# Kernel tuning notes

Hardware: AMD Instinct MI355X
Metric: run time of the kernel (lower is better)

Reference implementation:

```python
import jax, jax.numpy as jnp
import numpy as np

B, T, D, H, BAND = 2, 4096, 512, 8, 16
LN_EPS = 1e-5


def setup_inputs() -> dict:
    key = jax.random.key(0)
    k0, k1, k2 = jax.random.split(key, 3)
    x = jax.random.normal(k0, (B, T, D), jnp.float32)
    # nn.MultiheadAttention params: packed in_proj [3D, D] and out_proj [D, D]
    w_in = jax.random.normal(k1, (3 * D, D), jnp.float32) * 0.02
    b_in = jnp.zeros((3 * D,), jnp.float32)
    w_out = jax.random.normal(k2, (D, D), jnp.float32) * 0.02
    b_out = jnp.zeros((D,), jnp.float32)
    ln_g = jnp.ones((D,), jnp.float32)
    ln_b = jnp.zeros((D,), jnp.float32)
    return dict(x=x, ln_g=ln_g, ln_b=ln_b, w_in=w_in, b_in=b_in,
                w_out=w_out, b_out=b_out)


def reference(x, ln_g, ln_b, w_in, b_in, w_out, b_out):
    Bq, Tq, Dq = x.shape
    dh = Dq // H
    # LayerNorm
    mu = jnp.mean(x, axis=-1, keepdims=True)
    var = jnp.mean(jnp.square(x - mu), axis=-1, keepdims=True)
    h = (x - mu) * jax.lax.rsqrt(var + LN_EPS) * ln_g + ln_b
    # packed QKV projection (torch Linear: y = h @ W^T + b)
    qkv = h @ w_in.T + b_in                      # [B, T, 3D]
    q, k, v = jnp.split(qkv, 3, axis=-1)
    to_heads = lambda a: a.reshape(Bq, Tq, H, dh).transpose(0, 2, 1, 3)  # [B,H,T,dh]
    q, k, v = to_heads(q), to_heads(k), to_heads(v)
    # band-gather: each query t attends to keys in [t-BAND, t+BAND]
    Wn = 2 * BAND + 1
    offs = jnp.arange(-BAND, BAND + 1)
    idx = jnp.arange(Tq)[:, None] + offs[None, :]          # [T, Wn]
    valid = (idx >= 0) & (idx < Tq)                        # [T, Wn]
    idx_c = jnp.clip(idx, 0, Tq - 1)
    k_win = k[:, :, idx_c]                                 # [B,H,T,Wn,dh]
    v_win = v[:, :, idx_c]                                 # [B,H,T,Wn,dh]
    scale = 1.0 / np.sqrt(dh).astype(np.float32)
    scores = jnp.einsum('bhtd,bhtwd->bhtw', q * scale, k_win)
    scores = jnp.where(valid[None, None], scores, -jnp.inf)
    p = jax.nn.softmax(scores, axis=-1)                    # [B,H,T,Wn]
    o = jnp.einsum('bhtw,bhtwd->bhtd', p, v_win)           # [B,H,T,dh]
    o = o.transpose(0, 2, 1, 3).reshape(Bq, Tq, Dq)
    y = o @ w_out.T + b_out
    return x + y
```

## Files before the change

### kernel.cpp

```cpp
#include <hip/hip_runtime.h>
#include <hip/hip_bf16.h>

#define T_ 4096
#define D_ 512
#define H_ 8
#define BAND 16
#define G1_K 512
#define G1_NT 8

typedef float f32x4 __attribute__((ext_vector_type(4)));
typedef __bf16 bf16x8 __attribute__((ext_vector_type(8)));
typedef unsigned short us8 __attribute__((ext_vector_type(8)));
typedef unsigned short us4 __attribute__((ext_vector_type(4)));

__device__ __forceinline__ unsigned short f2b(float f) {
  union { float f; unsigned u; } v; v.f = f;
  unsigned r = v.u + 0x7fffu + ((v.u >> 16) & 1u);
  return (unsigned short)(r >> 16);
}

__device__ __forceinline__ f32x4 mfma16(bf16x8 a, bf16x8 b, f32x4 c) {
  return __builtin_amdgcn_mfma_f32_16x16x32_bf16(a, b, c, 0, 0, 0);
}

#define GLD16(gp, lp) __builtin_amdgcn_global_load_lds( \
    (const __attribute__((address_space(1))) void*)(gp), \
    (__attribute__((address_space(3))) void*)(lp), 16, 0, 0)

__global__ __launch_bounds__(256) void prep_k(const float* __restrict__ x,
                                              const float* __restrict__ g,
                                              const float* __restrict__ bt,
                                              const float* __restrict__ win,
                                              const float* __restrict__ wout,
                                              unsigned short* __restrict__ h,
                                              unsigned short* __restrict__ winb,
                                              unsigned short* __restrict__ woutb) {
  int bx = blockIdx.x;
  if (bx >= 2048) {
    int i = (bx - 2048) * 256 + threadIdx.x;
    const int n1 = 3 * D_ * D_ / 4;
    if (i < n1) {
      float4 v = ((const float4*)win)[i];
      us4 o; o.x = f2b(v.x); o.y = f2b(v.y); o.z = f2b(v.z); o.w = f2b(v.w);
      ((us4*)winb)[i] = o;
    } else {
      int j = i - n1;
      float4 v = ((const float4*)wout)[j];
      us4 o; o.x = f2b(v.x); o.y = f2b(v.y); o.z = f2b(v.z); o.w = f2b(v.w);
      ((us4*)woutb)[j] = o;
    }
    return;
  }
  int wave = threadIdx.x >> 6, lane = threadIdx.x & 63;
  size_t row = (size_t)bx * 4 + wave;
  const float4* xr = (const float4*)(x + row * D_);
  float4 a = xr[lane * 2], b = xr[lane * 2 + 1];
  float s = a.x + a.y + a.z + a.w + b.x + b.y + b.z + b.w;
  #pragma unroll
  for (int o = 32; o; o >>= 1) s += __shfl_xor(s, o, 64);
  float mu = s * (1.0f / D_);
  float d0 = a.x - mu, d1 = a.y - mu, d2 = a.z - mu, d3 = a.w - mu;
  float d4 = b.x - mu, d5 = b.y - mu, d6 = b.z - mu, d7 = b.w - mu;
  float q = d0*d0 + d1*d1 + d2*d2 + d3*d3 + d4*d4 + d5*d5 + d6*d6 + d7*d7;
  #pragma unroll
  for (int o = 32; o; o >>= 1) q += __shfl_xor(q, o, 64);
  float rstd = rsqrtf(q * (1.0f / D_) + 1e-5f);
  const float4* gr = (const float4*)g;
  const float4* br = (const float4*)bt;
  float4 g0 = gr[lane * 2], g1 = gr[lane * 2 + 1];
  float4 b0 = br[lane * 2], b1 = br[lane * 2 + 1];
  us8 o8;
  o8[0] = f2b(d0 * rstd * g0.x + b0.x);
  o8[1] = f2b(d1 * rstd * g0.y + b0.y);
  o8[2] = f2b(d2 * rstd * g0.z + b0.z);
  o8[3] = f2b(d3 * rstd * g0.w + b0.w);
  o8[4] = f2b(d4 * rstd * g1.x + b1.x);
  o8[5] = f2b(d5 * rstd * g1.y + b1.y);
  o8[6] = f2b(d6 * rstd * g1.z + b1.z);
  o8[7] = f2b(d7 * rstd * g1.w + b1.w);
  *((us8*)(h + row * D_) + lane) = o8;
}

#define OPA 0
#define OPB 1

__device__ __forceinline__ void stg(const unsigned short* __restrict__ gb,
                                    unsigned short* lds, int slot, int op, int h, int tt,
                                    int rl0, int u0, int su) {
  #pragma unroll
  for (int j = 0; j < 2; ++j) {
    const unsigned short* g = gb + (size_t)(h * 128 + rl0 + 64 * j) * G1_K + tt * 64 + su;
    unsigned short* lp = lds + slot * 32768 + op * 16384 + h * 8192 + (rl0 + 64 * j) * 64 + u0 * 8;
    GLD16(g, lp);
  }
}

#define VMC4 asm volatile("s_waitcnt vmcnt(4)" ::: "memory")
#define VMC0 asm volatile("s_waitcnt vmcnt(0)" ::: "memory")

#define PHASE(SLOT, PH, STAGE_STMT, WAIT_STMT) do {                                        \
    if ((PH) == 0) {                                                                       \
      _Pragma("unroll") for (int nf = 0; nf < 4; ++nf) {                                   \
        breg[nf][0] = *(const bf16x8*)(lds + (SLOT)*32768 + boff + nf*1024 + swz0);        \
        breg[nf][1] = *(const bf16x8*)(lds + (SLOT)*32768 + boff + nf*1024 + swz1);        \
      }                                                                                    \
    }                                                                                      \
    bf16x8 a0k0 = *(const bf16x8*)(lds + (SLOT)*32768 + aoff + (2*(PH))*1024 + swz0);      \
    bf16x8 a0k1 = *(const bf16x8*)(lds + (SLOT)*32768 + aoff + (2*(PH))*1024 + swz1);      \
    bf16x8 a1k0 = *(const bf16x8*)(lds + (SLOT)*32768 + aoff + (2*(PH)+1)*1024 + swz0);    \
    bf16x8 a1k1 = *(const bf16x8*)(lds + (SLOT)*32768 + aoff + (2*(PH)+1)*1024 + swz1);    \
    STAGE_STMT;                                                                            \
    __builtin_amdgcn_s_barrier();                                                          \
    asm volatile("s_waitcnt lgkmcnt(0)" ::: "memory");                                     \
    __builtin_amdgcn_sched_barrier(0);                                                     \
    __builtin_amdgcn_s_setprio(1);                                                         \
    _Pragma("unroll") for (int nf = 0; nf < 4; ++nf) {                                     \
      acc[2*(PH)][nf]   = mfma16(a0k0, breg[nf][0], acc[2*(PH)][nf]);                      \
      acc[2*(PH)][nf]   = mfma16(a0k1, breg[nf][1], acc[2*(PH)][nf]);                      \
      acc[2*(PH)+1][nf] = mfma16(a1k0, breg[nf][0], acc[2*(PH)+1][nf]);                    \
      acc[2*(PH)+1][nf] = mfma16(a1k1, breg[nf][1], acc[2*(PH)+1][nf]);                    \
    }                                                                                      \
    __builtin_amdgcn_s_setprio(0);                                                         \
    __builtin_amdgcn_sched_barrier(0);                                                     \
    WAIT_STMT;                                                                             \
    __builtin_amdgcn_s_barrier();                                                          \
  } while (0)

__global__ __launch_bounds__(512, 2) void gemm_qkv8(const unsigned short* __restrict__ A,
                                                    const unsigned short* __restrict__ Bw,
                                                    const float* __restrict__ bias,
                                                    unsigned short* __restrict__ C) {
  extern __shared__ char smem[];
  unsigned short* lds = (unsigned short*)smem;
  int tid = threadIdx.x;
  int lane = tid & 63, wave = tid >> 6;
  int wm = wave >> 2, wn = wave & 3;
  int fr = lane & 15, fq = lane >> 4;
  int d = blockIdx.x;
  int l = (d & 7) * 24 + (d >> 3);
  int bm = l / 6, bn = l % 6;

  const unsigned short* Ag = A + (size_t)bm * 256 * G1_K;
  const unsigned short* Bg = Bw + (size_t)bn * 256 * G1_K;

  int rl0 = tid >> 3, u0 = tid & 7;
  int su = (u0 ^ (rl0 & 7)) * 8;

  int aoff = wm * 8192 + fr * 64;
  int boff = 16384 + (wn >> 1) * 8192 + ((wn & 1) * 64 + fr) * 64;
  int swz0 = (fq ^ (fr & 7)) * 8;
  int swz1 = ((4 + fq) ^ (fr & 7)) * 8;

  f32x4 acc[8][4] = {};
  bf16x8 breg[4][2];

  stg(Bg, lds, 0, OPB, 0, 0, rl0, u0, su);
  stg(Bg, lds, 0, OPB, 1, 0, rl0, u0, su);
  stg(Ag, lds, 0, OPA, 0, 0, rl0, u0, su);
  stg(Ag, lds, 0, OPA, 1, 0, rl0, u0, su);
  stg(Bg, lds, 1, OPB, 0, 1, rl0, u0, su);
  stg(Bg, lds, 1, OPB, 1, 1, rl0, u0, su);
  VMC4;
  __builtin_amdgcn_s_barrier();

  #pragma unroll 1
  for (int i = 0; i < 3; ++i) {
    int t = 2 * i;
    PHASE(0, 0, stg(Ag, lds, 1, OPA, 0, t + 1, rl0, u0, su), (void)0);
    PHASE(0, 1, stg(Ag, lds, 1, OPA, 1, t + 1, rl0, u0, su), (void)0);
    PHASE(0, 2, stg(Bg, lds, 0, OPB, 0, t + 2, rl0, u0, su), (void)0);
    PHASE(0, 3, stg(Bg, lds, 0, OPB, 1, t + 2, rl0, u0, su), VMC4);
    PHASE(1, 0, stg(Ag, lds, 0, OPA, 0, t + 2, rl0, u0, su), (void)0);
    PHASE(1, 1, stg(Ag, lds, 0, OPA, 1, t + 2, rl0, u0, su), (void)0);
    PHASE(1, 2, stg(Bg, lds, 1, OPB, 0, t + 3, rl0, u0, su), (void)0);
    PHASE(1, 3, stg(Bg, lds, 1, OPB, 1, t + 3, rl0, u0, su), VMC4);
  }
  PHASE(0, 0, stg(Ag, lds, 1, OPA, 0, 7, rl0, u0, su), (void)0);
  PHASE(0, 1, stg(Ag, lds, 1, OPA, 1, 7, rl0, u0, su), (void)0);
  PHASE(0, 2, (void)0, (void)0);
  PHASE(0, 3, (void)0, VMC0);
  PHASE(1, 0, (void)0, (void)0);
  PHASE(1, 1, (void)0, (void)0);
  PHASE(1, 2, (void)0, (void)0);
  PHASE(1, 3, (void)0, (void)0);

  int rbase = bm * 256 + wm * 128 + fq * 4;
  int cbase = bn * 256 + wn * 64 + fr;
  float bv[4];
  #pragma unroll
  for (int nf = 0; nf < 4; ++nf) bv[nf] = bias[cbase + nf * 16];
  #pragma unroll
  for (int mf = 0; mf < 8; ++mf)
    #pragma unroll
    for (int nf = 0; nf < 4; ++nf)
      #pragma unroll
      for (int r = 0; r < 4; ++r)
        C[(size_t)(rbase + mf * 16 + r) * 1536 + cbase + nf * 16] = f2b(acc[mf][nf][r] + bv[nf]);
}

__global__ __launch_bounds__(256) void gemm_bt2(const unsigned short* __restrict__ A,
                                                const unsigned short* __restrict__ Bw,
                                                const float* __restrict__ bias,
                                                const float* __restrict__ xres,
                                                float* __restrict__ ofp,
                                                int N, int K) {
  __shared__ unsigned short As[128 * 64];
  __shared__ unsigned short Bs[128 * 64];
  int tid = threadIdx.x;
  int lane = tid & 63;
  int wave = tid >> 6;
  int wm = wave >> 1, wn = wave & 1;
  int fr = lane & 15, fq = lane >> 4;
  int dd = blockIdx.x;
  int nbn = N >> 7;
  int l = (dd & 7) * (gridDim.x >> 3) + (dd >> 3);
  int bm = l / nbn, bn = l % nbn;

  const unsigned short* Ap[4];
  const unsigned short* Bp[4];
  int loff[4];
  #pragma unroll
  for (int g = 0; g < 4; ++g) {
    int s = g * 256 + tid;
    int row = s >> 3, u = s & 7;
    int uu = u ^ (row & 7);
    Ap[g] = A + (size_t)(bm * 128 + row) * K + uu * 8;
    Bp[g] = Bw + (size_t)(bn * 128 + row) * K + uu * 8;
    loff[g] = s * 16;
  }

  f32x4 acc[4][4] = {};

  int nk = K >> 6;
  for (int kt = 0; kt < nk; ++kt) {
    int ko = kt * 64;
    #pragma unroll
    for (int g = 0; g < 4; ++g) GLD16(Ap[g] + ko, (char*)As + loff[g]);
    #pragma unroll
    for (int g = 0; g < 4; ++g) GLD16(Bp[g] + ko, (char*)Bs + loff[g]);
    __syncthreads();
    #pragma unroll
    for (int kk = 0; kk < 2; ++kk) {
      bf16x8 af[4], bfr[4];
      #pragma unroll
      for (int i = 0; i < 4; ++i) {
        int row = wm * 64 + i * 16 + fr;
        af[i] = *(const bf16x8*)(As + row * 64 + (((kk * 4 + fq) ^ (fr & 7)) << 3));
      }
      #pragma unroll
      for (int j = 0; j < 4; ++j) {
        int row = wn * 64 + j * 16 + fr;
        bfr[j] = *(const bf16x8*)(Bs + row * 64 + (((kk * 4 + fq) ^ (fr & 7)) << 3));
      }
      #pragma unroll
      for (int i = 0; i < 4; ++i)
        #pragma unroll
        for (int j = 0; j < 4; ++j)
          acc[i][j] = mfma16(af[i], bfr[j], acc[i][j]);
    }
    __syncthreads();
  }

  int rbase = bm * 128 + wm * 64 + fq * 4;
  int cb = bn * 128 + wn * 64 + fr;
  #pragma unroll
  for (int j = 0; j < 4; ++j) {
    int col = cb + j * 16;
    float bvv = bias[col];
    #pragma unroll
    for (int i = 0; i < 4; ++i) {
      #pragma unroll
      for (int r = 0; r < 4; ++r) {
        size_t idx = (size_t)(rbase + i * 16 + r) * N + col;
        ofp[idx] = xres[idx] + acc[i][j][r] + bvv;
      }
    }
  }
}

__global__ __launch_bounds__(256) void attn_k(const unsigned short* __restrict__ qkv,
                                              unsigned short* __restrict__ obuf) {
  __shared__ unsigned short Ks[96 * 72];
  __shared__ unsigned short Vt[64 * 128];
  __shared__ unsigned short Ps[64 * 104];
  int tid = threadIdx.x;
  int lane = tid & 63, wave = tid >> 6;
  int fr = lane & 15, fq = lane >> 4;
  int t0 = blockIdx.x * 64;
  int hh = blockIdx.y;
  int bb = blockIdx.z;
  size_t rowbase = (size_t)bb * T_;

  #pragma unroll
  for (int it = 0; it < 3; ++it) {
    int c = tid + it * 256;
    int r = c >> 3;
    int u = c & 7;
    int d8 = u * 8;
    int tg = t0 - BAND + r;
    us8 kv = {0,0,0,0,0,0,0,0}, vv = {0,0,0,0,0,0,0,0};
    if (tg >= 0 && tg < T_) {
      const unsigned short* p = qkv + (rowbase + tg) * 1536 + hh * 64 + d8;
      kv = *(const us8*)(p + 512);
      vv = *(const us8*)(p + 1024);
    }
    *(us8*)(Ks + r * 72 + d8) = kv;
    int ru = r >> 3, rl = r & 7;
    #pragma unroll
    for (int j = 0; j < 8; ++j)
      Vt[(d8 + j) * 128 + (((ru ^ u) << 3) | rl)] = vv[j];
  }

  bf16x8 qf0, qf1;
  {
    int tq = t0 + wave * 16 + fr;
    const unsigned short* qp = qkv + (rowbase + tq) * 1536 + hh * 64 + fq * 8;
    qf0 = *(const bf16x8*)qp;
    qf1 = *(const bf16x8*)(qp + 32);
  }
  __syncthreads();

  f32x4 sa[6];
  #pragma unroll
  for (int c = 0; c < 6; ++c) sa[c] = (f32x4){0.f, 0.f, 0.f, 0.f};
  #pragma unroll
  for (int c = 0; c < 6; ++c) {
    bf16x8 k0 = *(const bf16x8*)(Ks + (c * 16 + fr) * 72 + fq * 8);
    bf16x8 k1 = *(const bf16x8*)(Ks + (c * 16 + fr) * 72 + 32 + fq * 8);
    sa[c] = mfma16(qf0, k0, sa[c]);
    sa[c] = mfma16(qf1, k1, sa[c]);
  }

  float inv[4];
  float pvv[6][4];
  #pragma unroll
  for (int r = 0; r < 4; ++r) {
    int tg = t0 + wave * 16 + fq * 4 + r;
    float m = -1e30f;
    #pragma unroll
    for (int c = 0; c < 6; ++c) {
      int cg = t0 - BAND + c * 16 + fr;
      bool ok = (cg >= tg - BAND) && (cg <= tg + BAND) && (cg >= 0) && (cg < T_);
      float v = ok ? sa[c][r] * 0.125f : -1e30f;
      pvv[c][r] = v;
      m = fmaxf(m, v);
    }
    #pragma unroll
    for (int o = 8; o; o >>= 1) m = fmaxf(m, __shfl_xor(m, o, 64));
    float s = 0.0f;
    #pragma unroll
    for (int c = 0; c < 6; ++c) {
      float e = exp2f((pvv[c][r] - m) * 1.44269504f);
      pvv[c][r] = e;
      s += e;
    }
    #pragma unroll
    for (int o = 8; o; o >>= 1) s += __shfl_xor(s, o, 64);
    inv[r] = 1.0f / s;
  }

  #pragma unroll
  for (int c = 0; c < 6; ++c)
    #pragma unroll
    for (int r = 0; r < 4; ++r)
      Ps[(wave * 16 + fq * 4 + r) * 104 + c * 16 + fr] = f2b(pvv[c][r]);

  __syncthreads();

  f32x4 oa[4];
  #pragma unroll
  for (int c2 = 0; c2 < 4; ++c2) oa[c2] = (f32x4){0.f, 0.f, 0.f, 0.f};
  #pragma unroll
  for (int kk = 0; kk < 3; ++kk) {
    bf16x8 pa = *(const bf16x8*)(Ps + (wave * 16 + fr) * 104 + kk * 32 + fq * 8);
    #pragma unroll
    for (int c2 = 0; c2 < 4; ++c2) {
      int drow = c2 * 16 + fr;
      int ud = (drow >> 3) & 7;
      bf16x8 vb = *(const bf16x8*)(Vt + drow * 128 + (((kk * 4 + fq) ^ ud) << 3));
      oa[c2] = mfma16(pa, vb, oa[c2]);
    }
  }

  size_t orow = rowbase + t0 + wave * 16 + fq * 4;
  #pragma unroll
  for (int c2 = 0; c2 < 4; ++c2)
    #pragma unroll
    for (int r = 0; r < 4; ++r)
      obuf[(orow + r) * D_ + hh * 64 + c2 * 16 + fr] = f2b(oa[c2][r] * inv[r]);
}

extern "C" void kernel_launch(void* const* d_in, const int* in_sizes, int n_in,
                              void* d_out, int out_size, void* d_ws, size_t ws_size,
                              hipStream_t stream) {
  (void)in_sizes; (void)n_in; (void)out_size; (void)ws_size;
  const float* x     = (const float*)d_in[0];
  const float* ln_g  = (const float*)d_in[1];
  const float* ln_b  = (const float*)d_in[2];
  const float* w_in  = (const float*)d_in[3];
  const float* b_in  = (const float*)d_in[4];
  const float* w_out = (const float*)d_in[5];
  const float* b_out = (const float*)d_in[6];
  float* out = (float*)d_out;

  char* ws = (char*)d_ws;
  unsigned short* hb    = (unsigned short*)(ws);
  unsigned short* winb  = (unsigned short*)(ws + 8388608);
  unsigned short* woutb = (unsigned short*)(ws + 9961472);
  unsigned short* qkvb  = (unsigned short*)(ws + 10485760);
  unsigned short* obf   = (unsigned short*)(ws + 35651584);

  (void)hipFuncSetAttribute((const void*)gemm_qkv8,
                            hipFuncAttributeMaxDynamicSharedMemorySize, 131072);

  prep_k<<<3072, 256, 0, stream>>>(x, ln_g, ln_b, w_in, w_out, hb, winb, woutb);
  gemm_qkv8<<<192, 512, 131072, stream>>>(hb, winb, b_in, qkvb);
  attn_k<<<dim3(64, 8, 2), 256, 0, stream>>>(qkvb, obf);
  gemm_bt2<<<256, 256, 0, stream>>>(obf, woutb, b_out, x, out, 512, 512);
}
```

Before: 61.93 us.

## Fuse banded attention with output projection into one kernel

Replaces the separate attention kernel and output-projection GEMM with one kernel. Each block of 32 rows computes attention for all 8 heads, two passes of 4 heads each, into an LDS tile, then multiplies that tile by W_out with B fragments read straight from global memory. The residual add and bias are applied in the same kernel. This removes the bf16 attention-output round trip through global memory and one kernel launch. In exchange, each block redundantly reloads the K/V halo, and with only 256 blocks of 512 threads using about 114KB of LDS, parallelism and occupancy are lower.

New measurement: 61.77 us. No clear change (-0.3%).

```diff
diff --git a/kernel.cpp b/kernel.cpp
--- a/kernel.cpp
+++ b/kernel.cpp
@@ -6,7 +6,6 @@
 #define H_ 8
 #define BAND 16
 #define G1_K 512
-#define G1_NT 8
 
 typedef float f32x4 __attribute__((ext_vector_type(4)));
 typedef __bf16 bf16x8 __attribute__((ext_vector_type(8)));
@@ -198,196 +197,168 @@
         C[(size_t)(rbase + mf * 16 + r) * 1536 + cbase + nf * 16] = f2b(acc[mf][nf][r] + bv[nf]);
 }
 
-__global__ __launch_bounds__(256) void gemm_bt2(const unsigned short* __restrict__ A,
-                                                const unsigned short* __restrict__ Bw,
-                                                const float* __restrict__ bias,
-                                                const float* __restrict__ xres,
-                                                float* __restrict__ ofp,
-                                                int N, int K) {
-  __shared__ unsigned short As[128 * 64];
-  __shared__ unsigned short Bs[128 * 64];
-  int tid = threadIdx.x;
-  int lane = tid & 63;
-  int wave = tid >> 6;
-  int wm = wave >> 1, wn = wave & 1;
-  int fr = lane & 15, fq = lane >> 4;
-  int dd = blockIdx.x;
-  int nbn = N >> 7;
-  int l = (dd & 7) * (gridDim.x >> 3) + (dd >> 3);
-  int bm = l / nbn, bn = l % nbn;
-
-  const unsigned short* Ap[4];
-  const unsigned short* Bp[4];
-  int loff[4];
-  #pragma unroll
-  for (int g = 0; g < 4; ++g) {
-    int s = g * 256 + tid;
-    int row = s >> 3, u = s & 7;
-    int uu = u ^ (row & 7);
-    Ap[g] = A + (size_t)(bm * 128 + row) * K + uu * 8;
-    Bp[g] = Bw + (size_t)(bn * 128 + row) * K + uu * 8;
-    loff[g] = s * 16;
-  }
-
-  f32x4 acc[4][4] = {};
-
-  int nk = K >> 6;
-  for (int kt = 0; kt < nk; ++kt) {
-    int ko = kt * 64;
-    #pragma unroll
-    for (int g = 0; g < 4; ++g) GLD16(Ap[g] + ko, (char*)As + loff[g]);
-    #pragma unroll
-    for (int g = 0; g < 4; ++g) GLD16(Bp[g] + ko, (char*)Bs + loff[g]);
-    __syncthreads();
-    #pragma unroll
-    for (int kk = 0; kk < 2; ++kk) {
-      bf16x8 af[4], bfr[4];
-      #pragma unroll
-      for (int i = 0; i < 4; ++i) {
-        int row = wm * 64 + i * 16 + fr;
-        af[i] = *(const bf16x8*)(As + row * 64 + (((kk * 4 + fq) ^ (fr & 7)) << 3));
-      }
-      #pragma unroll
-      for (int j = 0; j < 4; ++j) {
-        int row = wn * 64 + j * 16 + fr;
-        bfr[j] = *(const bf16x8*)(Bs + row * 64 + (((kk * 4 + fq) ^ (fr & 7)) << 3));
-      }
-      #pragma unroll
-      for (int i = 0; i < 4; ++i)
-        #pragma unroll
-        for (int j = 0; j < 4; ++j)
-          acc[i][j] = mfma16(af[i], bfr[j], acc[i][j]);
-    }
-    __syncthreads();
-  }
-
-  int rbase = bm * 128 + wm * 64 + fq * 4;
-  int cb = bn * 128 + wn * 64 + fr;
-  #pragma unroll
-  for (int j = 0; j < 4; ++j) {
-    int col = cb + j * 16;
-    float bvv = bias[col];
-    #pragma unroll
-    for (int i = 0; i < 4; ++i) {
-      #pragma unroll
-      for (int r = 0; r < 4; ++r) {
-        size_t idx = (size_t)(rbase + i * 16 + r) * N + col;
-        ofp[idx] = xres[idx] + acc[i][j][r] + bvv;
-      }
-    }
-  }
-}
-
-__global__ __launch_bounds__(256) void attn_k(const unsigned short* __restrict__ qkv,
-                                              unsigned short* __restrict__ obuf) {
-  __shared__ unsigned short Ks[96 * 72];
-  __shared__ unsigned short Vt[64 * 128];
-  __shared__ unsigned short Ps[64 * 104];
+__global__ __launch_bounds__(512, 2) void attn_out_k(const unsigned short* __restrict__ qkv,
+                                                     const unsigned short* __restrict__ woutb,
+                                                     const float* __restrict__ bout,
+                                                     const float* __restrict__ x,
+                                                     float* __restrict__ out) {
+  extern __shared__ char smem2[];
+  unsigned short* lds = (unsigned short*)smem2;
   int tid = threadIdx.x;
   int lane = tid & 63, wave = tid >> 6;
   int fr = lane & 15, fq = lane >> 4;
-  int t0 = blockIdx.x * 64;
-  int hh = blockIdx.y;
-  int bb = blockIdx.z;
+  int r0g = blockIdx.x * 32;
+  int bb = r0g >> 12;
+  int t0 = r0g & (T_ - 1);
   size_t rowbase = (size_t)bb * T_;
 
-  #pragma unroll
-  for (int it = 0; it < 3; ++it) {
-    int c = tid + it * 256;
-    int r = c >> 3;
-    int u = c & 7;
-    int d8 = u * 8;
-    int tg = t0 - BAND + r;
-    us8 kv = {0,0,0,0,0,0,0,0}, vv = {0,0,0,0,0,0,0,0};
-    if (tg >= 0 && tg < T_) {
-      const unsigned short* p = qkv + (rowbase + tg) * 1536 + hh * 64 + d8;
-      kv = *(const us8*)(p + 512);
-      vv = *(const us8*)(p + 1024);
-    }
-    *(us8*)(Ks + r * 72 + d8) = kv;
-    int ru = r >> 3, rl = r & 7;
-    #pragma unroll
-    for (int j = 0; j < 8; ++j)
-      Vt[(d8 + j) * 128 + (((ru ^ u) << 3) | rl)] = vv[j];
-  }
-
-  bf16x8 qf0, qf1;
-  {
-    int tq = t0 + wave * 16 + fr;
-    const unsigned short* qp = qkv + (rowbase + tq) * 1536 + hh * 64 + fq * 8;
-    qf0 = *(const bf16x8*)qp;
-    qf1 = *(const bf16x8*)(qp + 32);
-  }
-  __syncthreads();
-
-  f32x4 sa[6];
-  #pragma unroll
-  for (int c = 0; c < 6; ++c) sa[c] = (f32x4){0.f, 0.f, 0.f, 0.f};
-  #pragma unroll
-  for (int c = 0; c < 6; ++c) {
-    bf16x8 k0 = *(const bf16x8*)(Ks + (c * 16 + fr) * 72 + fq * 8);
-    bf16x8 k1 = *(const bf16x8*)(Ks + (c * 16 + fr) * 72 + 32 + fq * 8);
-    sa[c] = mfma16(qf0, k0, sa[c]);
-    sa[c] = mfma16(qf1, k1, sa[c]);
-  }
-
-  float inv[4];
-  float pvv[6][4];
-  #pragma unroll
-  for (int r = 0; r < 4; ++r) {
-    int tg = t0 + wave * 16 + fq * 4 + r;
-    float m = -1e30f;
-    #pragma unroll
-    for (int c = 0; c < 6; ++c) {
-      int cg = t0 - BAND + c * 16 + fr;
-      bool ok = (cg >= tg - BAND) && (cg <= tg + BAND) && (cg >= 0) && (cg < T_);
-      float v = ok ? sa[c][r] * 0.125f : -1e30f;
-      pvv[c][r] = v;
-      m = fmaxf(m, v);
-    }
-    #pragma unroll
-    for (int o = 8; o; o >>= 1) m = fmaxf(m, __shfl_xor(m, o, 64));
-    float s = 0.0f;
-    #pragma unroll
-    for (int c = 0; c < 6; ++c) {
-      float e = exp2f((pvv[c][r] - m) * 1.44269504f);
-      pvv[c][r] = e;
-      s += e;
-    }
-    #pragma unroll
-    for (int o = 8; o; o >>= 1) s += __shfl_xor(s, o, 64);
-    inv[r] = 1.0f / s;
-  }
-
-  #pragma unroll
-  for (int c = 0; c < 6; ++c)
-    #pragma unroll
-    for (int r = 0; r < 4; ++r)
-      Ps[(wave * 16 + fq * 4 + r) * 104 + c * 16 + fr] = f2b(pvv[c][r]);
-
-  __syncthreads();
-
-  f32x4 oa[4];
-  #pragma unroll
-  for (int c2 = 0; c2 < 4; ++c2) oa[c2] = (f32x4){0.f, 0.f, 0.f, 0.f};
-  #pragma unroll
-  for (int kk = 0; kk < 3; ++kk) {
-    bf16x8 pa = *(const bf16x8*)(Ps + (wave * 16 + fr) * 104 + kk * 32 + fq * 8);
-    #pragma unroll
-    for (int c2 = 0; c2 < 4; ++c2) {
-      int drow = c2 * 16 + fr;
-      int ud = (drow >> 3) & 7;
-      bf16x8 vb = *(const bf16x8*)(Vt + drow * 128 + (((kk * 4 + fq) ^ ud) << 3));
-      oa[c2] = mfma16(pa, vb, oa[c2]);
-    }
-  }
-
-  size_t orow = rowbase + t0 + wave * 16 + fq * 4;
-  #pragma unroll
-  for (int c2 = 0; c2 < 4; ++c2)
-    #pragma unroll
-    for (int r = 0; r < 4; ++r)
-      obuf[(orow + r) * D_ + hh * 64 + c2 * 16 + fr] = f2b(oa[c2][r] * inv[r]);
+  unsigned short* Ob = lds + 41984;
+
+  #pragma unroll 1
+  for (int rd = 0; rd < 2; ++rd) {
+    #pragma unroll
+    for (int i = 0; i < 8; ++i) {
+      int idx = i * 512 + tid;
+      int s   = idx >> 10;
+      int rem = idx & 1023;
+      int ten = rem >> 9;
+      int c   = rem & 511;
+      int r   = c >> 3, u = c & 7;
+      int hh  = 4 * rd + s;
+      int tg  = t0 - BAND + r;
+      us8 v8 = {0, 0, 0, 0, 0, 0, 0, 0};
+      if (tg >= 0 && tg < T_)
+        v8 = *(const us8*)(qkv + (rowbase + tg) * 1536 + (ten ? 1024 : 512) + hh * 64 + u * 8);
+      if (ten == 0) {
+        *(us8*)(lds + s * 8192 + r * 64 + ((u ^ (r & 7)) << 3)) = v8;
+      } else {
+        int base = s * 8192 + 4096;
+        #pragma unroll
+        for (int j = 0; j < 8; ++j)
+          lds[base + (u * 8 + j) * 64 + (((r >> 3) ^ u) << 3) + (r & 7)] = v8[j];
+      }
+    }
+    __syncthreads();
+
+    {
+      int s  = wave >> 1;
+      int hh = 4 * rd + s;
+      int qg = wave & 1;
+      int q  = t0 + qg * 16 + fr;
+
+      const unsigned short* qp = qkv + (rowbase + q) * 1536 + hh * 64;
+      bf16x8 qf0 = *(const bf16x8*)(qp + fq * 8);
+      bf16x8 qf1 = *(const bf16x8*)(qp + 32 + fq * 8);
+
+      const unsigned short* Kb = lds + s * 8192;
+      f32x4 sacc[4];
+      #pragma unroll
+      for (int mf = 0; mf < 4; ++mf) sacc[mf] = (f32x4){0.f, 0.f, 0.f, 0.f};
+      #pragma unroll
+      for (int mf = 0; mf < 4; ++mf) {
+        bf16x8 k0 = *(const bf16x8*)(Kb + (mf * 16 + fr) * 64 + ((fq ^ (fr & 7)) << 3));
+        bf16x8 k1 = *(const bf16x8*)(Kb + (mf * 16 + fr) * 64 + (((4 + fq) ^ (fr & 7)) << 3));
+        sacc[mf] = mfma16(k0, qf0, sacc[mf]);
+        sacc[mf] = mfma16(k1, qf1, sacc[mf]);
+      }
+
+      float ev[4][4];
+      float vmx = -1e30f;
+      #pragma unroll
+      for (int mf = 0; mf < 4; ++mf)
+        #pragma unroll
+        for (int r = 0; r < 4; ++r) {
+          int tk = t0 - BAND + mf * 16 + fq * 4 + r;
+          bool ok = (tk >= q - BAND) && (tk <= q + BAND) && (tk >= 0) && (tk < T_);
+          float v = ok ? sacc[mf][r] * 0.125f : -1e30f;
+          ev[mf][r] = v;
+          vmx = fmaxf(vmx, v);
+        }
+      vmx = fmaxf(vmx, __shfl_xor(vmx, 16, 64));
+      vmx = fmaxf(vmx, __shfl_xor(vmx, 32, 64));
+      float ssum = 0.f;
+      #pragma unroll
+      for (int mf = 0; mf < 4; ++mf)
+        #pragma unroll
+        for (int r = 0; r < 4; ++r) {
+          float e = (ev[mf][r] > -1e29f) ? exp2f((ev[mf][r] - vmx) * 1.44269504f) : 0.f;
+          ev[mf][r] = e;
+          ssum += e;
+        }
+      ssum += __shfl_xor(ssum, 16, 64);
+      ssum += __shfl_xor(ssum, 32, 64);
+      float inv = 1.0f / ssum;
+
+      unsigned short* Pb = lds + 32768 + wave * 1152;
+      #pragma unroll
+      for (int mf = 0; mf < 4; ++mf)
+        #pragma unroll
+        for (int r = 0; r < 4; ++r)
+          Pb[fr * 72 + mf * 16 + fq * 4 + r] = f2b(ev[mf][r] * inv);
+      asm volatile("s_waitcnt lgkmcnt(0)" ::: "memory");
+      __builtin_amdgcn_sched_barrier(0);
+
+      const unsigned short* Vb = lds + s * 8192 + 4096;
+      f32x4 oacc[4];
+      #pragma unroll
+      for (int cf = 0; cf < 4; ++cf) oacc[cf] = (f32x4){0.f, 0.f, 0.f, 0.f};
+      #pragma unroll
+      for (int kk = 0; kk < 2; ++kk) {
+        bf16x8 pa = *(const bf16x8*)(Pb + fr * 72 + (kk * 4 + fq) * 8);
+        #pragma unroll
+        for (int cf = 0; cf < 4; ++cf) {
+          int du = cf * 2 + (fr >> 3);
+          bf16x8 vf = *(const bf16x8*)(Vb + (cf * 16 + fr) * 64 + (((kk * 4 + fq) ^ du) << 3));
+          oacc[cf] = mfma16(pa, vf, oacc[cf]);
+        }
+      }
+
+      #pragma unroll
+      for (int cf = 0; cf < 4; ++cf)
+        #pragma unroll
+        for (int r = 0; r < 4; ++r) {
+          int qq = qg * 16 + fq * 4 + r;
+          int unit = hh * 8 + (((cf * 2 + (fr >> 3)) ^ (qq & 7)));
+          Ob[qq * 512 + unit * 8 + (fr & 7)] = f2b(oacc[cf][r]);
+        }
+    }
+    __syncthreads();
+  }
+
+  f32x4 acc[2][4];
+  #pragma unroll
+  for (int mf = 0; mf < 2; ++mf)
+    #pragma unroll
+    for (int nf = 0; nf < 4; ++nf) acc[mf][nf] = (f32x4){0.f, 0.f, 0.f, 0.f};
+
+  const unsigned short* Bb = woutb + (size_t)(wave * 64) * 512;
+  #pragma unroll 4
+  for (int ks = 0; ks < 16; ++ks) {
+    bf16x8 a0 = *(const bf16x8*)(Ob + (0 * 16 + fr) * 512 + (((ks * 4 + fq) ^ (fr & 7)) << 3));
+    bf16x8 a1 = *(const bf16x8*)(Ob + (1 * 16 + fr) * 512 + (((ks * 4 + fq) ^ (fr & 7)) << 3));
+    bf16x8 bfr[4];
+    #pragma unroll
+    for (int nf = 0; nf < 4; ++nf)
+      bfr[nf] = *(const bf16x8*)(Bb + (size_t)(nf * 16 + fr) * 512 + ks * 32 + fq * 8);
+    #pragma unroll
+    for (int nf = 0; nf < 4; ++nf) {
+      acc[0][nf] = mfma16(a0, bfr[nf], acc[0][nf]);
+      acc[1][nf] = mfma16(a1, bfr[nf], acc[1][nf]);
+    }
+  }
+
+  #pragma unroll
+  for (int mf = 0; mf < 2; ++mf)
+    #pragma unroll
+    for (int nf = 0; nf < 4; ++nf) {
+      int col = wave * 64 + nf * 16 + fr;
+      float bv = bout[col];
+      #pragma unroll
+      for (int r = 0; r < 4; ++r) {
+        size_t e = (size_t)(r0g + mf * 16 + fq * 4 + r) * 512 + col;
+        out[e] = x[e] + acc[mf][nf][r] + bv;
+      }
+    }
 }
 
 extern "C" void kernel_launch(void* const* d_in, const int* in_sizes, int n_in,
@@ -408,13 +379,13 @@
   unsigned short* winb  = (unsigned short*)(ws + 8388608);
   unsigned short* woutb = (unsigned short*)(ws + 9961472);
   unsigned short* qkvb  = (unsigned short*)(ws + 10485760);
-  unsigned short* obf   = (unsigned short*)(ws + 35651584);
 
   (void)hipFuncSetAttribute((const void*)gemm_qkv8,
                             hipFuncAttributeMaxDynamicSharedMemorySize, 131072);
+  (void)hipFuncSetAttribute((const void*)attn_out_k,
+                            hipFuncAttributeMaxDynamicSharedMemorySize, 116736);
 
   prep_k<<<3072, 256, 0, stream>>>(x, ln_g, ln_b, w_in, w_out, hb, winb, woutb);
   gemm_qkv8<<<192, 512, 131072, stream>>>(hb, winb, b_in, qkvb);
-  attn_k<<<dim3(64, 8, 2), 256, 0, stream>>>(qkvb, obf);
-  gemm_bt2<<<256, 256, 0, stream>>>(obf, woutb, b_out, x, out, 512, 512);
-}
+  attn_out_k<<<256, 512, 116736, stream>>>(qkvb, woutb, b_out, x, out);
+}
```

## Retile QKV GEMM to 256x192 tiles for 256 blocks; simplify attention V layout

Applied to the files above, without the earlier changes.

The QKV GEMM tile changes from 256x256 to 256x192, so the grid grows from 192 to 256 blocks and fills all 256 CUs of the MI355X. B staging, the LDS slot size, the vmcnt waits and the block-to-tile mapping are reworked to match. Each block now does less MFMA work per staged A tile, which lowers arithmetic intensity. Separately, the attention kernel drops the XOR-swizzled transposed V layout for a padded stride-104 layout and adds an occupancy hint, which may introduce LDS bank conflicts.

Result: faster. 56.62 us (-8.6%).

```diff
diff --git a/kernel.cpp b/kernel.cpp
--- a/kernel.cpp
+++ b/kernel.cpp
@@ -6,7 +6,6 @@
 #define H_ 8
 #define BAND 16
 #define G1_K 512
-#define G1_NT 8
 
 typedef float f32x4 __attribute__((ext_vector_type(4)));
 typedef __bf16 bf16x8 __attribute__((ext_vector_type(8)));
@@ -81,40 +80,47 @@
   *((us8*)(h + row * D_) + lane) = o8;
 }
 
-#define OPA 0
-#define OPB 1
-
-__device__ __forceinline__ void stg(const unsigned short* __restrict__ gb,
-                                    unsigned short* lds, int slot, int op, int h, int tt,
-                                    int rl0, int u0, int su) {
+#define SLOT_SZ 28672
+
+__device__ __forceinline__ void stgA(const unsigned short* __restrict__ gb,
+                                     unsigned short* lds, int slot, int h, int tt,
+                                     int rl0, int u0, int su) {
   #pragma unroll
   for (int j = 0; j < 2; ++j) {
-    const unsigned short* g = gb + (size_t)(h * 128 + rl0 + 64 * j) * G1_K + tt * 64 + su;
-    unsigned short* lp = lds + slot * 32768 + op * 16384 + h * 8192 + (rl0 + 64 * j) * 64 + u0 * 8;
-    GLD16(g, lp);
-  }
-}
-
-#define VMC4 asm volatile("s_waitcnt vmcnt(4)" ::: "memory")
+    int row = h * 128 + rl0 + 64 * j;
+    GLD16(gb + (size_t)row * G1_K + tt * 64 + su, lds + slot * SLOT_SZ + row * 64 + u0 * 8);
+  }
+}
+__device__ __forceinline__ void stgB(const unsigned short* __restrict__ gb,
+                                     unsigned short* lds, int slot, int tt,
+                                     int rl0, int u0, int su) {
+  #pragma unroll
+  for (int c = 0; c < 3; ++c) {
+    int row = c * 64 + rl0;
+    GLD16(gb + (size_t)row * G1_K + tt * 64 + su, lds + slot * SLOT_SZ + 16384 + row * 64 + u0 * 8);
+  }
+}
+
+#define VMC3 asm volatile("s_waitcnt vmcnt(3)" ::: "memory")
 #define VMC0 asm volatile("s_waitcnt vmcnt(0)" ::: "memory")
 
 #define PHASE(SLOT, PH, STAGE_STMT, WAIT_STMT) do {                                        \
     if ((PH) == 0) {                                                                       \
-      _Pragma("unroll") for (int nf = 0; nf < 4; ++nf) {                                   \
-        breg[nf][0] = *(const bf16x8*)(lds + (SLOT)*32768 + boff + nf*1024 + swz0);        \
-        breg[nf][1] = *(const bf16x8*)(lds + (SLOT)*32768 + boff + nf*1024 + swz1);        \
+      _Pragma("unroll") for (int nf = 0; nf < 3; ++nf) {                                   \
+        breg[nf][0] = *(const bf16x8*)(lds + (SLOT)*SLOT_SZ + boff + nf*1024 + swz0);      \
+        breg[nf][1] = *(const bf16x8*)(lds + (SLOT)*SLOT_SZ + boff + nf*1024 + swz1);      \
       }                                                                                    \
     }                                                                                      \
-    bf16x8 a0k0 = *(const bf16x8*)(lds + (SLOT)*32768 + aoff + (2*(PH))*1024 + swz0);      \
-    bf16x8 a0k1 = *(const bf16x8*)(lds + (SLOT)*32768 + aoff + (2*(PH))*1024 + swz1);      \
-    bf16x8 a1k0 = *(const bf16x8*)(lds + (SLOT)*32768 + aoff + (2*(PH)+1)*1024 + swz0);    \
-    bf16x8 a1k1 = *(const bf16x8*)(lds + (SLOT)*32768 + aoff + (2*(PH)+1)*1024 + swz1);    \
+    bf16x8 a0k0 = *(const bf16x8*)(lds + (SLOT)*SLOT_SZ + aoff + (2*(PH))*1024 + swz0);    \
+    bf16x8 a0k1 = *(const bf16x8*)(lds + (SLOT)*SLOT_SZ + aoff + (2*(PH))*1024 + swz1);    \
+    bf16x8 a1k0 = *(const bf16x8*)(lds + (SLOT)*SLOT_SZ + aoff + (2*(PH)+1)*1024 + swz0);  \
+    bf16x8 a1k1 = *(const bf16x8*)(lds + (SLOT)*SLOT_SZ + aoff + (2*(PH)+1)*1024 + swz1);  \
     STAGE_STMT;                                                                            \
     __builtin_amdgcn_s_barrier();                                                          \
     asm volatile("s_waitcnt lgkmcnt(0)" ::: "memory");                                     \
     __builtin_amdgcn_sched_barrier(0);                                                     \
     __builtin_amdgcn_s_setprio(1);                                                         \
-    _Pragma("unroll") for (int nf = 0; nf < 4; ++nf) {                                     \
+    _Pragma("unroll") for (int nf = 0; nf < 3; ++nf) {                                     \
       acc[2*(PH)][nf]   = mfma16(a0k0, breg[nf][0], acc[2*(PH)][nf]);                      \
       acc[2*(PH)][nf]   = mfma16(a0k1, breg[nf][1], acc[2*(PH)][nf]);                      \
       acc[2*(PH)+1][nf] = mfma16(a1k0, breg[nf][0], acc[2*(PH)+1][nf]);                    \
@@ -137,46 +143,44 @@
   int wm = wave >> 2, wn = wave & 3;
   int fr = lane & 15, fq = lane >> 4;
   int d = blockIdx.x;
-  int l = (d & 7) * 24 + (d >> 3);
-  int bm = l / 6, bn = l % 6;
+  int l = (d & 7) * 32 + (d >> 3);
+  int bm = l >> 3, bn = l & 7;
 
   const unsigned short* Ag = A + (size_t)bm * 256 * G1_K;
-  const unsigned short* Bg = Bw + (size_t)bn * 256 * G1_K;
+  const unsigned short* Bg = Bw + (size_t)bn * 192 * G1_K;
 
   int rl0 = tid >> 3, u0 = tid & 7;
   int su = (u0 ^ (rl0 & 7)) * 8;
 
   int aoff = wm * 8192 + fr * 64;
-  int boff = 16384 + (wn >> 1) * 8192 + ((wn & 1) * 64 + fr) * 64;
+  int boff = 16384 + (wn * 48 + fr) * 64;
   int swz0 = (fq ^ (fr & 7)) * 8;
   int swz1 = ((4 + fq) ^ (fr & 7)) * 8;
 
-  f32x4 acc[8][4] = {};
-  bf16x8 breg[4][2];
-
-  stg(Bg, lds, 0, OPB, 0, 0, rl0, u0, su);
-  stg(Bg, lds, 0, OPB, 1, 0, rl0, u0, su);
-  stg(Ag, lds, 0, OPA, 0, 0, rl0, u0, su);
-  stg(Ag, lds, 0, OPA, 1, 0, rl0, u0, su);
-  stg(Bg, lds, 1, OPB, 0, 1, rl0, u0, su);
-  stg(Bg, lds, 1, OPB, 1, 1, rl0, u0, su);
-  VMC4;
+  f32x4 acc[8][3] = {};
+  bf16x8 breg[3][2];
+
+  stgB(Bg, lds, 0, 0, rl0, u0, su);
+  stgA(Ag, lds, 0, 0, 0, rl0, u0, su);
+  stgA(Ag, lds, 0, 1, 0, rl0, u0, su);
+  stgB(Bg, lds, 1, 1, rl0, u0, su);
+  VMC3;
   __builtin_amdgcn_s_barrier();
 
   #pragma unroll 1
   for (int i = 0; i < 3; ++i) {
     int t = 2 * i;
-    PHASE(0, 0, stg(Ag, lds, 1, OPA, 0, t + 1, rl0, u0, su), (void)0);
-    PHASE(0, 1, stg(Ag, lds, 1, OPA, 1, t + 1, rl0, u0, su), (void)0);
-    PHASE(0, 2, stg(Bg, lds, 0, OPB, 0, t + 2, rl0, u0, su), (void)0);
-    PHASE(0, 3, stg(Bg, lds, 0, OPB, 1, t + 2, rl0, u0, su), VMC4);
-    PHASE(1, 0, stg(Ag, lds, 0, OPA, 0, t + 2, rl0, u0, su), (void)0);
-    PHASE(1, 1, stg(Ag, lds, 0, OPA, 1, t + 2, rl0, u0, su), (void)0);
-    PHASE(1, 2, stg(Bg, lds, 1, OPB, 0, t + 3, rl0, u0, su), (void)0);
-    PHASE(1, 3, stg(Bg, lds, 1, OPB, 1, t + 3, rl0, u0, su), VMC4);
-  }
-  PHASE(0, 0, stg(Ag, lds, 1, OPA, 0, 7, rl0, u0, su), (void)0);
-  PHASE(0, 1, stg(Ag, lds, 1, OPA, 1, 7, rl0, u0, su), (void)0);
+    PHASE(0, 0, stgA(Ag, lds, 1, 0, t + 1, rl0, u0, su), (void)0);
+    PHASE(0, 1, stgA(Ag, lds, 1, 1, t + 1, rl0, u0, su), (void)0);
+    PHASE(0, 2, stgB(Bg, lds, 0, t + 2, rl0, u0, su), (void)0);
+    PHASE(0, 3, (void)0, VMC3);
+    PHASE(1, 0, stgA(Ag, lds, 0, 0, t + 2, rl0, u0, su), (void)0);
+    PHASE(1, 1, stgA(Ag, lds, 0, 1, t + 2, rl0, u0, su), (void)0);
+    PHASE(1, 2, stgB(Bg, lds, 1, t + 3, rl0, u0, su), (void)0);
+    PHASE(1, 3, (void)0, VMC3);
+  }
+  PHASE(0, 0, stgA(Ag, lds, 1, 0, 7, rl0, u0, su), (void)0);
+  PHASE(0, 1, stgA(Ag, lds, 1, 1, 7, rl0, u0, su), (void)0);
   PHASE(0, 2, (void)0, (void)0);
   PHASE(0, 3, (void)0, VMC0);
   PHASE(1, 0, (void)0, (void)0);
@@ -185,14 +189,14 @@
   PHASE(1, 3, (void)0, (void)0);
 
   int rbase = bm * 256 + wm * 128 + fq * 4;
-  int cbase = bn * 256 + wn * 64 + fr;
-  float bv[4];
-  #pragma unroll
-  for (int nf = 0; nf < 4; ++nf) bv[nf] = bias[cbase + nf * 16];
+  int cbase = bn * 192 + wn * 48 + fr;
+  float bv[3];
+  #pragma unroll
+  for (int nf = 0; nf < 3; ++nf) bv[nf] = bias[cbase + nf * 16];
   #pragma unroll
   for (int mf = 0; mf < 8; ++mf)
     #pragma unroll
-    for (int nf = 0; nf < 4; ++nf)
+    for (int nf = 0; nf < 3; ++nf)
       #pragma unroll
       for (int r = 0; r < 4; ++r)
         C[(size_t)(rbase + mf * 16 + r) * 1536 + cbase + nf * 16] = f2b(acc[mf][nf][r] + bv[nf]);
@@ -278,10 +282,10 @@
   }
 }
 
-__global__ __launch_bounds__(256) void attn_k(const unsigned short* __restrict__ qkv,
-                                              unsigned short* __restrict__ obuf) {
+__global__ __launch_bounds__(256, 4) void attn_k(const unsigned short* __restrict__ qkv,
+                                                 unsigned short* __restrict__ obuf) {
   __shared__ unsigned short Ks[96 * 72];
-  __shared__ unsigned short Vt[64 * 128];
+  __shared__ unsigned short Vt[64 * 104];
   __shared__ unsigned short Ps[64 * 104];
   int tid = threadIdx.x;
   int lane = tid & 63, wave = tid >> 6;
@@ -305,10 +309,8 @@
       vv = *(const us8*)(p + 1024);
     }
     *(us8*)(Ks + r * 72 + d8) = kv;
-    int ru = r >> 3, rl = r & 7;
-    #pragma unroll
-    for (int j = 0; j < 8; ++j)
-      Vt[(d8 + j) * 128 + (((ru ^ u) << 3) | rl)] = vv[j];
+    #pragma unroll
+    for (int j = 0; j < 8; ++j) Vt[(d8 + j) * 104 + r] = vv[j];
   }
 
   bf16x8 qf0, qf1;
@@ -375,9 +377,7 @@
     bf16x8 pa = *(const bf16x8*)(Ps + (wave * 16 + fr) * 104 + kk * 32 + fq * 8);
     #pragma unroll
     for (int c2 = 0; c2 < 4; ++c2) {
-      int drow = c2 * 16 + fr;
-      int ud = (drow >> 3) & 7;
-      bf16x8 vb = *(const bf16x8*)(Vt + drow * 128 + (((kk * 4 + fq) ^ ud) << 3));
+      bf16x8 vb = *(const bf16x8*)(Vt + (c2 * 16 + fr) * 104 + kk * 32 + fq * 8);
       oa[c2] = mfma16(pa, vb, oa[c2]);
     }
   }
@@ -411,10 +411,10 @@
   unsigned short* obf   = (unsigned short*)(ws + 35651584);
 
   (void)hipFuncSetAttribute((const void*)gemm_qkv8,
-                            hipFuncAttributeMaxDynamicSharedMemorySize, 131072);
+                            hipFuncAttributeMaxDynamicSharedMemorySize, 114688);
 
   prep_k<<<3072, 256, 0, stream>>>(x, ln_g, ln_b, w_in, w_out, hb, winb, woutb);
-  gemm_qkv8<<<192, 512, 131072, stream>>>(hb, winb, b_in, qkvb);
+  gemm_qkv8<<<256, 512, 114688, stream>>>(hb, winb, b_in, qkvb);
   attn_k<<<dim3(64, 8, 2), 256, 0, stream>>>(qkvb, obf);
   gemm_bt2<<<256, 256, 0, stream>>>(obf, woutb, b_out, x, out, 512, 512);
 }
```
